# Kernel tuning notes

Hardware: AMD Instinct MI355X
Metric: run time of the kernel (lower is better)

Reference implementation:

```python
import jax, jax.numpy as jnp
import numpy as np

E, M, T, H, V = 512, 1024, 1024, 512, 10000
B, S, L = 16, 80, 200
K = 10  # pooling kernel


def avgpool2d(x, k):
    # torch AvgPool2d(k) on a 3D tensor [B, S, C]: pools over (S, C) with stride k, floor mode
    b, s, c = x.shape
    return x[:, :(s // k) * k, :(c // k) * k].reshape(b, s // k, k, c // k, k).mean(axis=(2, 4))


def lstm(x, h0, c0, Wih, Whh, bih, bhh):
    # torch single-layer LSTM, gate order (i, f, g, o); x: [B, T, H]
    def step(carry, xt):
        h, c = carry
        g = xt @ Wih.T + h @ Whh.T + bih + bhh  # [B, 4H]
        i, f, gg, o = jnp.split(g, 4, axis=-1)
        c = jax.nn.sigmoid(f) * c + jax.nn.sigmoid(i) * jnp.tanh(gg)
        h = jax.nn.sigmoid(o) * jnp.tanh(c)
        return (h, c), h
    (hT, cT), ys = jax.lax.scan(step, (h0, c0), jnp.swapaxes(x, 0, 1))
    return jnp.swapaxes(ys, 0, 1), (hT, cT)


def attend(emb, feats, lens, Ws, bs, hdim):
    # additive score: Linear(cat(emb, feat)) = emb@We.T + feat@Wf.T + b, masked softmax over valid feats
    we, wf = Ws[:, :hdim], Ws[:, hdim:]
    scores = emb @ we.T + jnp.swapaxes(feats @ wf.T, 1, 2) + bs  # [B, S, L]
    mask = jnp.arange(feats.shape[1])[None, None, :] < lens[:, None, None]
    w = jax.nn.softmax(jnp.where(mask, scores, -jnp.inf), axis=-1)
    return jnp.einsum('bsl,blf->bsf', w, feats)


def setup_inputs():
    key = jax.random.key(0)
    ks = jax.random.split(key, 30)
    n = lambda k, shape: jax.random.normal(k, shape, dtype=jnp.float32)
    p = lambda k, shape: 0.02 * jax.random.normal(k, shape, dtype=jnp.float32)
    inp = {
        'mfeat': n(ks[0], (B, L, M)),
        'tfeat': n(ks[1], (B, L, T)),
        'att_motion': n(ks[2], (B, S, M)),
        'att_tempo': n(ks[3], (B, S, T)),
        'embeddings': n(ks[4], (B, S, E)),
        'motion_batch_lens': jax.random.randint(ks[5], (B,), 100, L + 1, dtype=jnp.int32),
        'temp_batch_lens': jax.random.randint(ks[6], (B,), 100, L + 1, dtype=jnp.int32),
        'seq_batch_lens': jnp.full((B,), S, dtype=jnp.int32),
        'Wm': p(ks[7], (M, M)), 'bm': p(ks[8], (M,)),
        'Wt': p(ks[9], (T, T)), 'bt': p(ks[10], (T,)),
        'Wmm': p(ks[11], (H, E + T + M)), 'bmm': p(ks[12], (H,)),
        'Wli': p(ks[13], (H, T // K + M // K)), 'bli': p(ks[14], (H,)),
        'Wih': p(ks[15], (4 * H, H)), 'Whh': p(ks[16], (4 * H, H)),
        'bih': p(ks[17], (4 * H,)), 'bhh': p(ks[18], (4 * H,)),
        'Wsm': p(ks[19], (1, H + M)), 'bsm': p(ks[20], (1,)),
        'Wst': p(ks[21], (1, H + T)), 'bst': p(ks[22], (1,)),
        'Wo': p(ks[23], (V, H + T + M)), 'bo': p(ks[24], (V,)),
    }
    return inp


def reference(mfeat, tfeat, att_motion, att_tempo, embeddings,
              motion_batch_lens, temp_batch_lens, seq_batch_lens,
              Wm, bm, Wt, bt, Wmm, bmm, Wli, bli,
              Wih, Whh, bih, bhh, Wsm, bsm, Wst, bst, Wo, bo):
    # self-gated feature transforms
    temp_mout = att_motion @ Wm.T + bm
    temp_tout = att_tempo @ Wt.T + bt
    temp_mout = temp_mout * jax.nn.softmax(temp_mout, axis=-1)
    temp_tout = temp_tout * jax.nn.softmax(temp_tout, axis=-1)
    # multimodal fusion (dropout = identity in eval)
    mm_inp = jnp.concatenate((embeddings, temp_tout, temp_mout), axis=2)
    mm_out = mm_inp @ Wmm.T + bmm  # [B, S, H]
    # pooled init sequence -> LSTM init hidden
    mean_feat = jnp.concatenate((avgpool2d(att_tempo, K), avgpool2d(att_motion, K)), axis=2)
    m0 = mean_feat @ Wli.T + bli  # [B, S//K, H]
    z = jnp.zeros((att_motion.shape[0], H), dtype=mm_out.dtype)
    _, (h0, c0) = lstm(m0, z, z, Wih, Whh, bih, bhh)
    out, _ = lstm(mm_out, h0, c0, Wih, Whh, bih, bhh)
    act = jnp.tanh(out)
    # ragged additive attention over variable-length video features
    att_m2 = attend(act, mfeat, motion_batch_lens, Wsm, bsm, H)
    att_t2 = attend(act, tfeat, temp_batch_lens, Wst, bst, H)
    final = jnp.concatenate((act, att_t2, att_m2), axis=2) @ Wo.T + bo
    return jax.nn.log_softmax(final, axis=2)
```

## Files before the change

### kernel.cpp

```cpp
#include <hip/hip_runtime.h>
#include <hip/hip_bf16.h>
#include <math.h>


typedef __bf16 bf16x8 __attribute__((ext_vector_type(8)));
typedef float f32x4 __attribute__((ext_vector_type(4)));
typedef unsigned short u16x8 __attribute__((ext_vector_type(8)));

__device__ inline unsigned short f2b(float f){
  union { float f; unsigned u; } v; v.f = f;
  unsigned u = v.u;
  u += 0x7fff + ((u >> 16) & 1);
  return (unsigned short)(u >> 16);
}
__device__ inline float sigm(float x){ return 1.f/(1.f + __expf(-x)); }
__device__ inline float wred_max(float v){ for (int o=32;o;o>>=1) v = fmaxf(v, __shfl_xor(v,o)); return v; }
__device__ inline float wred_sum(float v){ for (int o=32;o;o>>=1) v += __shfl_xor(v,o); return v; }

__device__ inline float bred_max(float v, float* sm){
  v = wred_max(v);
  int w = threadIdx.x >> 6;
  if ((threadIdx.x & 63) == 0) sm[w] = v;
  __syncthreads();
  v = fmaxf(fmaxf(sm[0], sm[1]), fmaxf(sm[2], sm[3]));
  __syncthreads();
  return v;
}
__device__ inline float bred_sum(float v, float* sm){
  v = wred_sum(v);
  int w = threadIdx.x >> 6;
  if ((threadIdx.x & 63) == 0) sm[w] = v;
  __syncthreads();
  v = sm[0] + sm[1] + sm[2] + sm[3];
  __syncthreads();
  return v;
}

#define GLOAD_LDS16(g, l) __builtin_amdgcn_global_load_lds( \
    (const __attribute__((address_space(1))) void*)(g), \
    (__attribute__((address_space(3))) void*)(l), 16, 0, 0)

__global__ void cvt_bf16_kernel(const float* __restrict__ s, unsigned short* __restrict__ d, int n8){
  int i = blockIdx.x*256 + threadIdx.x;
  if (i >= n8) return;
  float4 a = ((const float4*)s)[i*2];
  float4 b = ((const float4*)s)[i*2+1];
  u16x8 o;
  o[0]=f2b(a.x); o[1]=f2b(a.y); o[2]=f2b(a.z); o[3]=f2b(a.w);
  o[4]=f2b(b.x); o[5]=f2b(b.y); o[6]=f2b(b.z); o[7]=f2b(b.w);
  ((u16x8*)d)[i] = o;
}

__global__ void zero_kernel(int* p, int n){
  int i = blockIdx.x*64 + threadIdx.x;
  if (i < n) p[i] = 0;
}

__global__ __launch_bounds__(256) void gemm_bb_kernel(
    const unsigned short* __restrict__ A, const unsigned short* __restrict__ B,
    const float* __restrict__ bias1, const float* __restrict__ bias2,
    float* __restrict__ C, int N, int K)
{
  __shared__ unsigned short lA[128*32];
  __shared__ unsigned short lB[128*32];
  int tid = threadIdx.x;
  int r0 = blockIdx.x << 7, n0 = blockIdx.y << 7;
  int w = tid >> 6, lane = tid & 63;
  int wr = (w >> 1) << 6, wc = (w & 1) << 6;
  int lm = lane & 15, lq = lane >> 4;
  f32x4 acc[4][4] = {};

  int row0 = tid >> 2, row1 = (tid + 256) >> 2, cc = (tid & 3) << 3;
  const unsigned short* Ag0 = A + (size_t)(r0 + row0)*K + cc;
  const unsigned short* Ag1 = A + (size_t)(r0 + row1)*K + cc;
  int br0 = n0 + row0; if (br0 >= N) br0 = N - 1;
  int br1 = n0 + row1; if (br1 >= N) br1 = N - 1;
  const unsigned short* Bg0 = B + (size_t)br0*K + cc;
  const unsigned short* Bg1 = B + (size_t)br1*K + cc;
  unsigned lb0 = (unsigned)(tid & ~63) * 8;
  unsigned lb1 = 2048 + lb0;

  for (int k0 = 0; k0 < K; k0 += 32){
    GLOAD_LDS16(Ag0 + k0, &lA[lb0]);
    GLOAD_LDS16(Ag1 + k0, &lA[lb1]);
    GLOAD_LDS16(Bg0 + k0, &lB[lb0]);
    GLOAD_LDS16(Bg1 + k0, &lB[lb1]);
    __syncthreads();
    bf16x8 af[4], bfr[4];
#pragma unroll
    for (int i=0;i<4;i++){
      af[i]  = *(const bf16x8*)&lA[(wr + i*16 + lm)*32 + lq*8];
      bfr[i] = *(const bf16x8*)&lB[(wc + i*16 + lm)*32 + lq*8];
    }
#pragma unroll
    for (int i=0;i<4;i++)
#pragma unroll
      for (int j=0;j<4;j++)
        acc[i][j] = __builtin_amdgcn_mfma_f32_16x16x32_bf16(af[i], bfr[j], acc[i][j], 0, 0, 0);
    __syncthreads();
  }
#pragma unroll
  for (int i=0;i<4;i++){
    int rbase = r0 + wr + i*16 + lq*4;
#pragma unroll
    for (int j=0;j<4;j++){
      int n = n0 + wc + j*16 + lm;
      if (n < N){
        float bv = (bias1 ? bias1[n] : 0.f) + (bias2 ? bias2[n] : 0.f);
#pragma unroll
        for (int rr=0;rr<4;rr++)
          C[(size_t)(rbase + rr)*N + n] = acc[i][j][rr] + bv;
      }
    }
  }
}

__global__ __launch_bounds__(256) void rowsmx_kernel(const float* __restrict__ X,
    unsigned short* __restrict__ out, int ostride, int ooff)
{
  __shared__ float sm[4];
  int row = blockIdx.x, tid = threadIdx.x;
  const float* xr = X + (size_t)row * 1024;
  float x[4];
#pragma unroll
  for (int j=0;j<4;j++) x[j] = xr[j*256 + tid];
  float m = fmaxf(fmaxf(x[0],x[1]), fmaxf(x[2],x[3]));
  m = bred_max(m, sm);
  float s = 0.f;
#pragma unroll
  for (int j=0;j<4;j++) s += __expf(x[j]-m);
  s = bred_sum(s, sm);
  float inv = 1.f / s;
  unsigned short* o = out + (size_t)row*ostride + ooff;
#pragma unroll
  for (int j=0;j<4;j++) o[j*256 + tid] = f2b(x[j] * (__expf(x[j]-m) * inv));
}

__global__ void embcopy_kernel(const float* __restrict__ emb, unsigned short* __restrict__ mmbf){
  int idx = blockIdx.x*256 + threadIdx.x;
  if (idx >= 1280*64) return;
  int row = idx >> 6, c8 = (idx & 63) << 3;
  const float* s = emb + (size_t)row*512 + c8;
  float4 a = ((const float4*)s)[0], b = ((const float4*)s)[1];
  u16x8 o;
  o[0]=f2b(a.x); o[1]=f2b(a.y); o[2]=f2b(a.z); o[3]=f2b(a.w);
  o[4]=f2b(b.x); o[5]=f2b(b.y); o[6]=f2b(b.z); o[7]=f2b(b.w);
  *(u16x8*)&mmbf[(size_t)row*2560 + c8] = o;
}

__global__ void avgpool_kernel(const float* __restrict__ tempo, const float* __restrict__ motion,
                               float* __restrict__ mf)
{
  int bx = blockIdx.x;
  int c = threadIdx.x;
  if (c >= 204) return;
  int b = bx >> 3, s = bx & 7;
  const float* src = (c < 102) ? (tempo  + ((size_t)(b*80 + s*10))*1024 + c*10)
                               : (motion + ((size_t)(b*80 + s*10))*1024 + (c-102)*10);
  float acc = 0.f;
  for (int r=0;r<10;r++){
    const float* p = src + (size_t)r*1024;
#pragma unroll
    for (int cc=0;cc<10;cc++) acc += p[cc];
  }
  mf[bx*204 + c] = acc * 0.01f;
}

__global__ __launch_bounds__(256) void m0_kernel(const float* __restrict__ mf,
    const float* __restrict__ Wli, const float* __restrict__ bli, float* __restrict__ m0)
{
  __shared__ float rowv[204];
  int bx = blockIdx.x, tid = threadIdx.x;
  if (tid < 204) rowv[tid] = mf[bx*204 + tid];
  __syncthreads();
  for (int c = tid; c < 512; c += 256){
    const float* w = Wli + (size_t)c*204;
    float acc = bli[c];
    for (int k=0;k<204;k++) acc += rowv[k]*w[k];
    m0[bx*512 + c] = acc;
  }
}

#define LSTM_NBLK 32
#define HP 520

__global__ __launch_bounds__(256) void lstm_fused_kernel(
    const float* __restrict__ X1, const float* __restrict__ X2,
    const float* __restrict__ Whh,
    unsigned long long* __restrict__ hb0, unsigned long long* __restrict__ hb1,
    float* __restrict__ finalA, int* __restrict__ bar)
{
  __shared__ unsigned short w_lds[64*HP];
  __shared__ unsigned short h_lds[16*HP];
  __shared__ float gb[4][16][16];
  __shared__ unsigned short hstage[16][16];
  int tid = threadIdx.x, j = blockIdx.x;
  int j16 = j*16;
  int lane = tid & 63, w = tid >> 6;
  int lm = lane & 15, lq = lane >> 4;

  for (int i = 0; i < 16; i++){
    int ch = tid + i*256;
    int r = ch >> 6, c8 = (ch & 63) << 3;
    int grow = (r >> 4)*512 + j16 + (r & 15);
    const float* s = Whh + (size_t)grow*512 + c8;
    float4 a = ((const float4*)s)[0], b = ((const float4*)s)[1];
    u16x8 o;
    o[0]=f2b(a.x); o[1]=f2b(a.y); o[2]=f2b(a.z); o[3]=f2b(a.w);
    o[4]=f2b(b.x); o[5]=f2b(b.y); o[6]=f2b(b.z); o[7]=f2b(b.w);
    *(u16x8*)&w_lds[r*HP + c8] = o;
  }

  float c_reg = 0.f;
  int ul = tid & 15, bb = tid >> 4;
  unsigned long long* hbufs[2] = { hb0, hb1 };
  const int wbase = ((w << 4) + lm)*HP;
  const int abase = lm*HP;
  const int koff = lq << 3;
  int sc = 0;

  for (int seg = 0; seg < 2; seg++){
    const float* Xp = seg ? X2 : X1;
    int Tst = seg ? 80 : 8;
    for (int t = 0; t < Tst; t++){
      if (sc > 0){
        if (tid == 0){
          while (__hip_atomic_load(&bar[sc-1], __ATOMIC_RELAXED, __HIP_MEMORY_SCOPE_AGENT) < LSTM_NBLK)
            __builtin_amdgcn_s_sleep(1);
        }
        __syncthreads();
      }
      size_t xrow = ((size_t)bb*Tst + t)*2048 + j16 + ul;
      float xi = Xp[xrow];
      float xf = Xp[xrow + 512];
      float xg = Xp[xrow + 1024];
      float xo = Xp[xrow + 1536];
      if (sc == 0){
        u16x8 z = {0,0,0,0,0,0,0,0};
        for (int i = tid; i < 1024; i += 256){
          int b = i >> 6, c8 = (i & 63) << 3;
          *(u16x8*)&h_lds[b*HP + c8] = z;
        }
      } else {
        const unsigned long long* src = hbufs[sc & 1];
#pragma unroll
        for (int it = 0; it < 4; it++){
          int i = tid + it*256;
          int b = i >> 6, c64 = i & 63;
          unsigned long long v = __hip_atomic_load(&src[i], __ATOMIC_RELAXED, __HIP_MEMORY_SCOPE_AGENT);
          *(unsigned long long*)&h_lds[b*HP + (c64 << 2)] = v;
        }
      }
      __syncthreads();
      f32x4 a0 = {0.f,0.f,0.f,0.f}, a1 = {0.f,0.f,0.f,0.f};
#pragma unroll
      for (int k0 = 0; k0 < 512; k0 += 64){
        bf16x8 ha = *(const bf16x8*)&h_lds[abase + k0 + koff];
        bf16x8 wa = *(const bf16x8*)&w_lds[wbase + k0 + koff];
        a0 = __builtin_amdgcn_mfma_f32_16x16x32_bf16(ha, wa, a0, 0, 0, 0);
        bf16x8 hbf = *(const bf16x8*)&h_lds[abase + k0 + 32 + koff];
        bf16x8 wbf = *(const bf16x8*)&w_lds[wbase + k0 + 32 + koff];
        a1 = __builtin_amdgcn_mfma_f32_16x16x32_bf16(hbf, wbf, a1, 0, 0, 0);
      }
      f32x4 acc = a0 + a1;
      *(f32x4*)&gb[w][lm][lq << 2] = acc;
      __syncthreads();
      float iv = gb[0][ul][bb] + xi;
      float fv = gb[1][ul][bb] + xf;
      float gv = gb[2][ul][bb] + xg;
      float ov = gb[3][ul][bb] + xo;
      c_reg = sigm(fv)*c_reg + sigm(iv)*tanhf(gv);
      float hn = sigm(ov)*tanhf(c_reg);
      hstage[bb][ul] = f2b(hn);
      if (seg) finalA[(size_t)(bb*80 + t)*2560 + j16 + ul] = tanhf(hn);
      __syncthreads();
      if (tid < 64){
        int b = tid >> 2, ch = tid & 3;
        unsigned long long v = *(const unsigned long long*)&hstage[b][ch << 2];
        unsigned long long* dst = hbufs[(sc + 1) & 1] + (size_t)b*64 + (j16 >> 2) + ch;
        __hip_atomic_store(dst, v, __ATOMIC_RELAXED, __HIP_MEMORY_SCOPE_AGENT);
      }
      sc++;
      __syncthreads();
      if (tid == 0)
        __hip_atomic_fetch_add(&bar[sc-1], 1, __ATOMIC_RELAXED, __HIP_MEMORY_SCOPE_AGENT);
    }
  }
}

__global__ void proj_kernel(const float* __restrict__ A, int stride, int ncols,
                            const float* __restrict__ w, const float* __restrict__ bias,
                            float* __restrict__ out)
{
  int r = blockIdx.x, lane = threadIdx.x;
  const float* a = A + (size_t)r * stride;
  float acc = 0.f;
  for (int c = lane; c < ncols; c += 64) acc += a[c]*w[c];
  acc = wred_sum(acc);
  if (lane == 0) out[r] = acc + (bias ? bias[0] : 0.f);
}

__global__ __launch_bounds__(256) void attsmax_kernel(const float* __restrict__ e,
    const float* __restrict__ f, const int* __restrict__ lens, float* __restrict__ w)
{
  __shared__ float sm[4];
  int bx = blockIdx.x;
  int b = bx / 80;
  int tid = threadIdx.x;
  int len = lens[b];
  bool ok = (tid < 200) && (tid < len);
  float val = ok ? (e[bx] + f[b*200 + tid]) : -1e30f;
  float m = bred_max(val, sm);
  float ex = ok ? __expf(val - m) : 0.f;
  float s = bred_sum(ex, sm);
  if (tid < 200) w[(size_t)bx*200 + tid] = ex / s;
}

__global__ __launch_bounds__(256) void attapply_kernel(const float* __restrict__ w,
    const float* __restrict__ feats, float* __restrict__ finalA, int coloff)
{
  __shared__ float lw[8][200];
  int b = blockIdx.x, sg = blockIdx.y;
  int tid = threadIdx.x;
  for (int i = tid; i < 1600; i += 256){
    int ss = i / 200, l = i - ss*200;
    lw[ss][l] = w[(size_t)(b*80 + sg*8 + ss)*200 + l];
  }
  __syncthreads();
  float4 acc[8];
#pragma unroll
  for (int s=0;s<8;s++) acc[s] = make_float4(0,0,0,0);
  const float* fb = feats + (size_t)b*200*1024 + tid*4;
  for (int l=0;l<200;l++){
    float4 v = *(const float4*)(fb + (size_t)l*1024);
#pragma unroll
    for (int s=0;s<8;s++){
      float wv = lw[s][l];
      acc[s].x += wv*v.x; acc[s].y += wv*v.y; acc[s].z += wv*v.z; acc[s].w += wv*v.w;
    }
  }
#pragma unroll
  for (int s=0;s<8;s++){
    float* o = finalA + (size_t)(b*80 + sg*8 + s)*2560 + coloff + tid*4;
    *(float4*)o = acc[s];
  }
}

__global__ __launch_bounds__(256) void logsmax_kernel(float* __restrict__ out)
{
  __shared__ float buf[10000];
  __shared__ float sm[4];
  int row = blockIdx.x, tid = threadIdx.x;
  float* o = out + (size_t)row * 10000;
  float m = -1e30f;
  for (int i = tid; i < 10000; i += 256){ float v = o[i]; buf[i] = v; m = fmaxf(m, v); }
  m = bred_max(m, sm);
  float s = 0.f;
  for (int i = tid; i < 10000; i += 256) s += __expf(buf[i] - m);
  s = bred_sum(s, sm);
  float lse = m + __logf(s);
  for (int i = tid; i < 10000; i += 256) o[i] = buf[i] - lse;
}

extern "C" void kernel_launch(void* const* d_in, const int* in_sizes, int n_in,
                              void* d_out, int out_size, void* d_ws, size_t ws_size,
                              hipStream_t stream)
{
  const float* mfeat = (const float*)d_in[0];
  const float* tfeat = (const float*)d_in[1];
  const float* attm  = (const float*)d_in[2];
  const float* attt  = (const float*)d_in[3];
  const float* emb   = (const float*)d_in[4];
  const int* lens_m  = (const int*)d_in[5];
  const int* lens_t  = (const int*)d_in[6];
  const float* Wm  = (const float*)d_in[8];
  const float* bm  = (const float*)d_in[9];
  const float* Wt  = (const float*)d_in[10];
  const float* bt  = (const float*)d_in[11];
  const float* Wmm = (const float*)d_in[12];
  const float* bmm = (const float*)d_in[13];
  const float* Wli = (const float*)d_in[14];
  const float* bli = (const float*)d_in[15];
  const float* Wih = (const float*)d_in[16];
  const float* Whh = (const float*)d_in[17];
  const float* bih = (const float*)d_in[18];
  const float* bhh = (const float*)d_in[19];
  const float* Wsm = (const float*)d_in[20];
  const float* bsm = (const float*)d_in[21];
  const float* Wst = (const float*)d_in[22];
  const float* bst = (const float*)d_in[23];
  const float* Wo  = (const float*)d_in[24];
  const float* bo  = (const float*)d_in[25];
  float* out = (float*)d_out;

  char* ws = (char*)d_ws;
  size_t off = 0;
  auto alloc = [&](size_t bytes)->void* {
    void* p = (void*)(ws + off);
    off += (bytes + 255) & ~(size_t)255;
    return p;
  };
  float* finalA = (float*)alloc(1280UL*2560*4);
  float* moutp  = (float*)alloc(1280UL*1024*4);
  float* toutp  = (float*)alloc(1280UL*1024*4);
  float* mm_out = (float*)alloc(1280UL*512*4);
  float* meanf  = (float*)alloc(128UL*204*4);
  float* m0     = (float*)alloc(128UL*512*4);
  float* X1     = (float*)alloc(128UL*2048*4);
  float* X2     = (float*)alloc(1280UL*2048*4);
  float* e_m = (float*)alloc(1280UL*4); float* e_t = (float*)alloc(1280UL*4);
  float* f_m = (float*)alloc(3200UL*4); float* f_t = (float*)alloc(3200UL*4);
  float* w_m = (float*)alloc(1280UL*200*4); float* w_t = (float*)alloc(1280UL*200*4);
  int* bar = (int*)alloc(128*4);
  unsigned long long* hbuf0 = (unsigned long long*)alloc(16UL*512*2);
  unsigned long long* hbuf1 = (unsigned long long*)alloc(16UL*512*2);
  unsigned short* attm_bf   = (unsigned short*)alloc(1280UL*1024*2);
  unsigned short* attt_bf   = (unsigned short*)alloc(1280UL*1024*2);
  unsigned short* Wm_bf     = (unsigned short*)alloc(1024UL*1024*2);
  unsigned short* Wt_bf     = (unsigned short*)alloc(1024UL*1024*2);
  unsigned short* Wmm_bf    = (unsigned short*)alloc(512UL*2560*2);
  unsigned short* Wih_bf    = (unsigned short*)alloc(2048UL*512*2);
  unsigned short* Wo_bf     = (unsigned short*)alloc(10000UL*2560*2);
  unsigned short* mm_inp_bf = (unsigned short*)alloc(1280UL*2560*2);
  unsigned short* mm_out_bf = (unsigned short*)alloc(1280UL*512*2);
  unsigned short* m0_bf     = (unsigned short*)alloc(128UL*512*2);
  unsigned short* finalA_bf = (unsigned short*)alloc(1280UL*2560*2);

  auto cvt = [&](const float* s, unsigned short* d, size_t n){
    int n8 = (int)(n/8);
    cvt_bf16_kernel<<<(n8 + 255)/256, 256, 0, stream>>>(s, d, n8);
  };
  cvt(attm, attm_bf, 1280UL*1024);
  cvt(attt, attt_bf, 1280UL*1024);
  cvt(Wm,  Wm_bf,  1024UL*1024);
  cvt(Wt,  Wt_bf,  1024UL*1024);
  cvt(Wmm, Wmm_bf, 512UL*2560);
  cvt(Wih, Wih_bf, 2048UL*512);
  cvt(Wo,  Wo_bf,  10000UL*2560);
  zero_kernel<<<2, 64, 0, stream>>>(bar, 128);

  gemm_bb_kernel<<<dim3(10, 8), 256, 0, stream>>>(attm_bf, Wm_bf, bm, nullptr, moutp, 1024, 1024);
  gemm_bb_kernel<<<dim3(10, 8), 256, 0, stream>>>(attt_bf, Wt_bf, bt, nullptr, toutp, 1024, 1024);
  rowsmx_kernel<<<1280, 256, 0, stream>>>(moutp, mm_inp_bf, 2560, 1536);
  rowsmx_kernel<<<1280, 256, 0, stream>>>(toutp, mm_inp_bf, 2560, 512);
  embcopy_kernel<<<(1280*64 + 255)/256, 256, 0, stream>>>(emb, mm_inp_bf);
  gemm_bb_kernel<<<dim3(10, 4), 256, 0, stream>>>(mm_inp_bf, Wmm_bf, bmm, nullptr, mm_out, 512, 2560);
  cvt(mm_out, mm_out_bf, 1280UL*512);
  avgpool_kernel<<<128, 256, 0, stream>>>(attt, attm, meanf);
  m0_kernel<<<128, 256, 0, stream>>>(meanf, Wli, bli, m0);
  cvt(m0, m0_bf, 128UL*512);
  gemm_bb_kernel<<<dim3(1, 16), 256, 0, stream>>>(m0_bf, Wih_bf, bih, bhh, X1, 2048, 512);
  gemm_bb_kernel<<<dim3(10, 16), 256, 0, stream>>>(mm_out_bf, Wih_bf, bih, bhh, X2, 2048, 512);
  lstm_fused_kernel<<<LSTM_NBLK, 256, 0, stream>>>(X1, X2, Whh, hbuf0, hbuf1, finalA, bar);
  proj_kernel<<<1280, 64, 0, stream>>>(finalA, 2560, 512, Wsm, bsm, e_m);
  proj_kernel<<<3200, 64, 0, stream>>>(mfeat, 1024, 1024, Wsm + 512, nullptr, f_m);
  proj_kernel<<<1280, 64, 0, stream>>>(finalA, 2560, 512, Wst, bst, e_t);
  proj_kernel<<<3200, 64, 0, stream>>>(tfeat, 1024, 1024, Wst + 512, nullptr, f_t);
  attsmax_kernel<<<1280, 256, 0, stream>>>(e_t, f_t, lens_t, w_t);
  attsmax_kernel<<<1280, 256, 0, stream>>>(e_m, f_m, lens_m, w_m);
  attapply_kernel<<<dim3(16,10), 256, 0, stream>>>(w_t, tfeat, finalA, 512);
  attapply_kernel<<<dim3(16,10), 256, 0, stream>>>(w_m, mfeat, finalA, 1536);
  cvt(finalA, finalA_bf, 1280UL*2560);
  gemm_bb_kernel<<<dim3(10, 79), 256, 0, stream>>>(finalA_bf, Wo_bf, bo, nullptr, out, 10000, 2560);
  logsmax_kernel<<<1280, 256, 0, stream>>>(out);
}
```

Before: 1.044 ms.

## Use per-wave flag barriers and wave-local gate layout in fused LSTM

Reorders the Whh rows each block keeps in LDS so that every wave holds all four gates for four hidden units. Each wave can then apply the cell update from its own MFMA output without block-wide syncs. The shared atomic counter barrier becomes per-step, per-wave flags that every lane polls, h is packed with shuffles and published per wave, and the h LDS buffer is double-buffered. tanhf is also replaced with an exp-based fast tanh. This targets per-timestep latency in the serial recurrence, at the cost of more flag memory, more polling traffic, and slightly different tanh accuracy.

```diff
diff --git a/kernel.cpp b/kernel.cpp
--- a/kernel.cpp
+++ b/kernel.cpp
@@ -14,6 +14,10 @@
   return (unsigned short)(u >> 16);
 }
 __device__ inline float sigm(float x){ return 1.f/(1.f + __expf(-x)); }
+__device__ inline float tanh_fast(float x){
+  float e = __expf(2.f*x);
+  return 1.f - 2.f/(e + 1.f);
+}
 __device__ inline float wred_max(float v){ for (int o=32;o;o>>=1) v = fmaxf(v, __shfl_xor(v,o)); return v; }
 __device__ inline float wred_sum(float v){ for (int o=32;o;o>>=1) v += __shfl_xor(v,o); return v; }
 
@@ -191,18 +195,18 @@
     float* __restrict__ finalA, int* __restrict__ bar)
 {
   __shared__ unsigned short w_lds[64*HP];
-  __shared__ unsigned short h_lds[16*HP];
-  __shared__ float gb[4][16][16];
-  __shared__ unsigned short hstage[16][16];
+  __shared__ unsigned short h_lds[2][16*HP];
+  __shared__ float gbw[4][16][20];
   int tid = threadIdx.x, j = blockIdx.x;
   int j16 = j*16;
   int lane = tid & 63, w = tid >> 6;
   int lm = lane & 15, lq = lane >> 4;
+  int bc = lane >> 2, uu = lane & 3, ul = (w << 2) + uu;
 
   for (int i = 0; i < 16; i++){
     int ch = tid + i*256;
     int r = ch >> 6, c8 = (ch & 63) << 3;
-    int grow = (r >> 4)*512 + j16 + (r & 15);
+    int grow = ((r >> 2) & 3)*512 + j16 + ((r >> 4) << 2) + (r & 3);
     const float* s = Whh + (size_t)grow*512 + c8;
     float4 a = ((const float4*)s)[0], b = ((const float4*)s)[1];
     u16x8 o;
@@ -210,10 +214,15 @@
     o[4]=f2b(b.x); o[5]=f2b(b.y); o[6]=f2b(b.z); o[7]=f2b(b.w);
     *(u16x8*)&w_lds[r*HP + c8] = o;
   }
+  {
+    u16x8 z = {0,0,0,0,0,0,0,0};
+    for (int i = tid; i < 1024; i += 256){
+      int b = i >> 6, c8 = (i & 63) << 3;
+      *(u16x8*)&h_lds[0][b*HP + c8] = z;
+    }
+  }
 
   float c_reg = 0.f;
-  int ul = tid & 15, bb = tid >> 4;
-  unsigned long long* hbufs[2] = { hb0, hb1 };
   const int wbase = ((w << 4) + lm)*HP;
   const int abase = lm*HP;
   const int koff = lq << 3;
@@ -222,68 +231,65 @@
   for (int seg = 0; seg < 2; seg++){
     const float* Xp = seg ? X2 : X1;
     int Tst = seg ? 80 : 8;
-    for (int t = 0; t < Tst; t++){
-      if (sc > 0){
-        if (tid == 0){
-          while (__hip_atomic_load(&bar[sc-1], __ATOMIC_RELAXED, __HIP_MEMORY_SCOPE_AGENT) < LSTM_NBLK)
-            __builtin_amdgcn_s_sleep(1);
-        }
-        __syncthreads();
-      }
-      size_t xrow = ((size_t)bb*Tst + t)*2048 + j16 + ul;
+    for (int t = 0; t < Tst; t++, sc++){
+      bool last = (seg == 1) && (t == Tst - 1);
+      size_t xrow = ((size_t)bc*Tst + t)*2048 + j16 + ul;
       float xi = Xp[xrow];
       float xf = Xp[xrow + 512];
       float xg = Xp[xrow + 1024];
       float xo = Xp[xrow + 1536];
-      if (sc == 0){
-        u16x8 z = {0,0,0,0,0,0,0,0};
-        for (int i = tid; i < 1024; i += 256){
-          int b = i >> 6, c8 = (i & 63) << 3;
-          *(u16x8*)&h_lds[b*HP + c8] = z;
-        }
-      } else {
-        const unsigned long long* src = hbufs[sc & 1];
-#pragma unroll
-        for (int it = 0; it < 4; it++){
+      if (sc > 0){
+        const int* fp = bar + (sc - 1)*128;
+        while (__hip_atomic_load(&fp[lane], __ATOMIC_RELAXED, __HIP_MEMORY_SCOPE_AGENT) == 0)
+          __builtin_amdgcn_s_sleep(1);
+        while (__hip_atomic_load(&fp[lane + 64], __ATOMIC_RELAXED, __HIP_MEMORY_SCOPE_AGENT) == 0)
+          __builtin_amdgcn_s_sleep(1);
+        asm volatile("" ::: "memory");
+        const unsigned long long* src = (sc & 1) ? hb1 : hb0;
+        unsigned short* hb = &h_lds[sc & 1][0];
+#pragma unroll
+        for (int it = 0; it < 8; it++){
           int i = tid + it*256;
-          int b = i >> 6, c64 = i & 63;
+          int b = i >> 7, c64 = i & 127;
           unsigned long long v = __hip_atomic_load(&src[i], __ATOMIC_RELAXED, __HIP_MEMORY_SCOPE_AGENT);
-          *(unsigned long long*)&h_lds[b*HP + (c64 << 2)] = v;
+          *(unsigned long long*)&hb[b*HP + (c64 << 2)] = v;
         }
       }
       __syncthreads();
+      const unsigned short* hrow = &h_lds[sc & 1][abase];
       f32x4 a0 = {0.f,0.f,0.f,0.f}, a1 = {0.f,0.f,0.f,0.f};
 #pragma unroll
       for (int k0 = 0; k0 < 512; k0 += 64){
-        bf16x8 ha = *(const bf16x8*)&h_lds[abase + k0 + koff];
+        bf16x8 ha = *(const bf16x8*)&hrow[k0 + koff];
         bf16x8 wa = *(const bf16x8*)&w_lds[wbase + k0 + koff];
         a0 = __builtin_amdgcn_mfma_f32_16x16x32_bf16(ha, wa, a0, 0, 0, 0);
-        bf16x8 hbf = *(const bf16x8*)&h_lds[abase + k0 + 32 + koff];
+        bf16x8 hbf = *(const bf16x8*)&hrow[k0 + 32 + koff];
         bf16x8 wbf = *(const bf16x8*)&w_lds[wbase + k0 + 32 + koff];
         a1 = __builtin_amdgcn_mfma_f32_16x16x32_bf16(hbf, wbf, a1, 0, 0, 0);
       }
-      f32x4 acc = a0 + a1;
-      *(f32x4*)&gb[w][lm][lq << 2] = acc;
-      __syncthreads();
-      float iv = gb[0][ul][bb] + xi;
-      float fv = gb[1][ul][bb] + xf;
-      float gv = gb[2][ul][bb] + xg;
-      float ov = gb[3][ul][bb] + xo;
-      c_reg = sigm(fv)*c_reg + sigm(iv)*tanhf(gv);
-      float hn = sigm(ov)*tanhf(c_reg);
-      hstage[bb][ul] = f2b(hn);
-      if (seg) finalA[(size_t)(bb*80 + t)*2560 + j16 + ul] = tanhf(hn);
-      __syncthreads();
-      if (tid < 64){
-        int b = tid >> 2, ch = tid & 3;
-        unsigned long long v = *(const unsigned long long*)&hstage[b][ch << 2];
-        unsigned long long* dst = hbufs[(sc + 1) & 1] + (size_t)b*64 + (j16 >> 2) + ch;
-        __hip_atomic_store(dst, v, __ATOMIC_RELAXED, __HIP_MEMORY_SCOPE_AGENT);
+      *(f32x4*)&gbw[w][lm][lq << 2] = a0 + a1;
+      float iv = gbw[w][uu     ][bc] + xi;
+      float fv = gbw[w][4 + uu ][bc] + xf;
+      float gv = gbw[w][8 + uu ][bc] + xg;
+      float ov = gbw[w][12 + uu][bc] + xo;
+      c_reg = sigm(fv)*c_reg + sigm(iv)*tanh_fast(gv);
+      float hn = sigm(ov)*tanh_fast(c_reg);
+      if (seg) finalA[(size_t)(bc*80 + t)*2560 + j16 + ul] = tanh_fast(hn);
+      if (!last){
+        unsigned hv = (unsigned)f2b(hn);
+        unsigned p = (hv & 0xffffu) | ((unsigned)__shfl_xor((int)hv, 1) << 16);
+        unsigned q = (unsigned)__shfl_xor((int)p, 2);
+        if ((lane & 3) == 0){
+          unsigned long long v64 = ((unsigned long long)q << 32) | (unsigned long long)p;
+          unsigned long long* dstb = ((sc + 1) & 1) ? hb1 : hb0;
+          __hip_atomic_store(dstb + (size_t)bc*128 + (j << 2) + w, v64,
+                             __ATOMIC_RELAXED, __HIP_MEMORY_SCOPE_AGENT);
+        }
+        asm volatile("s_waitcnt vmcnt(0)" ::: "memory");
+        if (lane == 0)
+          __hip_atomic_store(&bar[sc*128 + (j << 2) + w], 1,
+                             __ATOMIC_RELAXED, __HIP_MEMORY_SCOPE_AGENT);
       }
-      sc++;
-      __syncthreads();
-      if (tid == 0)
-        __hip_atomic_fetch_add(&bar[sc-1], 1, __ATOMIC_RELAXED, __HIP_MEMORY_SCOPE_AGENT);
     }
   }
 }
@@ -411,7 +417,7 @@
   float* e_m = (float*)alloc(1280UL*4); float* e_t = (float*)alloc(1280UL*4);
   float* f_m = (float*)alloc(3200UL*4); float* f_t = (float*)alloc(3200UL*4);
   float* w_m = (float*)alloc(1280UL*200*4); float* w_t = (float*)alloc(1280UL*200*4);
-  int* bar = (int*)alloc(128*4);
+  int* bar = (int*)alloc(88UL*128*4);
   unsigned long long* hbuf0 = (unsigned long long*)alloc(16UL*512*2);
   unsigned long long* hbuf1 = (unsigned long long*)alloc(16UL*512*2);
   unsigned short* attm_bf   = (unsigned short*)alloc(1280UL*1024*2);
@@ -437,7 +443,7 @@
   cvt(Wmm, Wmm_bf, 512UL*2560);
   cvt(Wih, Wih_bf, 2048UL*512);
   cvt(Wo,  Wo_bf,  10000UL*2560);
-  zero_kernel<<<2, 64, 0, stream>>>(bar, 128);
+  zero_kernel<<<(88*128 + 63)/64, 64, 0, stream>>>(bar, 88*128);
 
   gemm_bb_kernel<<<dim3(10, 8), 256, 0, stream>>>(attm_bf, Wm_bf, bm, nullptr, moutp, 1024, 1024);
   gemm_bb_kernel<<<dim3(10, 8), 256, 0, stream>>>(attt_bf, Wt_bf, bt, nullptr, toutp, 1024, 1024);
```

Measured after the change: 1.284 ms. 1.23x slower.

## Overlap Wo bf16 conversion and feature projections with LSTM via extra blocks

Applied to the files above, without the earlier changes.

Launches 224 extra blocks alongside the 32 recurrent LSTM blocks. They convert Wo to bf16 and compute the mfeat/tfeat score projections while the latency-bound recurrence runs on otherwise idle CUs. The LSTM and attapply kernels now write bf16 finalA directly, which drops a separate conversion pass. Paired GEMMs and row-softmax launches are merged into single launches. The hidden-state exchange now reads the full 512-wide row, which the old loop did not. Extra blocks could compete for scheduling with the spin-barrier LSTM blocks.

```diff
diff --git a/kernel.cpp b/kernel.cpp
--- a/kernel.cpp
+++ b/kernel.cpp
@@ -56,13 +56,12 @@
   if (i < n) p[i] = 0;
 }
 
-__global__ __launch_bounds__(256) void gemm_bb_kernel(
+__device__ __forceinline__ void gemm_body(
     const unsigned short* __restrict__ A, const unsigned short* __restrict__ B,
     const float* __restrict__ bias1, const float* __restrict__ bias2,
-    float* __restrict__ C, int N, int K)
-{
-  __shared__ unsigned short lA[128*32];
-  __shared__ unsigned short lB[128*32];
+    float* __restrict__ C, int N, int K,
+    unsigned short* lA, unsigned short* lB)
+{
   int tid = threadIdx.x;
   int r0 = blockIdx.x << 7, n0 = blockIdx.y << 7;
   int w = tid >> 6, lane = tid & 63;
@@ -115,12 +114,36 @@
   }
 }
 
-__global__ __launch_bounds__(256) void rowsmx_kernel(const float* __restrict__ X,
-    unsigned short* __restrict__ out, int ostride, int ooff)
+__global__ __launch_bounds__(256) void gemm_bb_kernel(
+    const unsigned short* __restrict__ A, const unsigned short* __restrict__ B,
+    const float* __restrict__ bias1, const float* __restrict__ bias2,
+    float* __restrict__ C, int N, int K)
+{
+  __shared__ unsigned short lA[128*32];
+  __shared__ unsigned short lB[128*32];
+  gemm_body(A, B, bias1, bias2, C, N, K, lA, lB);
+}
+
+__global__ __launch_bounds__(256) void gemm_bb2_kernel(
+    const unsigned short* __restrict__ A0, const unsigned short* __restrict__ B0,
+    const float* __restrict__ b0, float* __restrict__ C0,
+    const unsigned short* __restrict__ A1, const unsigned short* __restrict__ B1,
+    const float* __restrict__ b1, float* __restrict__ C1, int N, int K)
+{
+  __shared__ unsigned short lA[128*32];
+  __shared__ unsigned short lB[128*32];
+  if (blockIdx.z == 0) gemm_body(A0, B0, b0, nullptr, C0, N, K, lA, lB);
+  else                 gemm_body(A1, B1, b1, nullptr, C1, N, K, lA, lB);
+}
+
+__global__ __launch_bounds__(256) void rowsmx2_kernel(const float* __restrict__ X0,
+    const float* __restrict__ X1, unsigned short* __restrict__ out)
 {
   __shared__ float sm[4];
-  int row = blockIdx.x, tid = threadIdx.x;
-  const float* xr = X + (size_t)row * 1024;
+  int bx = blockIdx.x, tid = threadIdx.x;
+  int row = (bx < 1280) ? bx : bx - 1280;
+  const float* xr = ((bx < 1280) ? X0 : X1) + (size_t)row * 1024;
+  int ooff = (bx < 1280) ? 1536 : 512;
   float x[4];
 #pragma unroll
   for (int j=0;j<4;j++) x[j] = xr[j*256 + tid];
@@ -131,7 +154,7 @@
   for (int j=0;j<4;j++) s += __expf(x[j]-m);
   s = bred_sum(s, sm);
   float inv = 1.f / s;
-  unsigned short* o = out + (size_t)row*ostride + ooff;
+  unsigned short* o = out + (size_t)row*2560 + ooff;
 #pragma unroll
   for (int j=0;j<4;j++) o[j*256 + tid] = f2b(x[j] * (__expf(x[j]-m) * inv));
 }
@@ -188,13 +211,42 @@
     const float* __restrict__ X1, const float* __restrict__ X2,
     const float* __restrict__ Whh,
     unsigned long long* __restrict__ hb0, unsigned long long* __restrict__ hb1,
-    float* __restrict__ finalA, int* __restrict__ bar)
+    float* __restrict__ finalA, unsigned short* __restrict__ finalA_bf,
+    int* __restrict__ bar,
+    const float* __restrict__ Wo, unsigned short* __restrict__ Wo_bf,
+    const float* __restrict__ mfeat, const float* __restrict__ tfeat,
+    const float* __restrict__ Wsm, const float* __restrict__ Wst,
+    float* __restrict__ f_m, float* __restrict__ f_t)
 {
   __shared__ unsigned short w_lds[64*HP];
   __shared__ unsigned short h_lds[16*HP];
   __shared__ float gb[4][16][16];
   __shared__ unsigned short hstage[16][16];
   int tid = threadIdx.x, j = blockIdx.x;
+
+  if (j >= LSTM_NBLK){
+    int hb = j - LSTM_NBLK;
+    for (int ch = hb*256 + tid; ch < 3200000; ch += 224*256){
+      float4 a = ((const float4*)Wo)[ch*2];
+      float4 b = ((const float4*)Wo)[ch*2+1];
+      u16x8 o;
+      o[0]=f2b(a.x); o[1]=f2b(a.y); o[2]=f2b(a.z); o[3]=f2b(a.w);
+      o[4]=f2b(b.x); o[5]=f2b(b.y); o[6]=f2b(b.z); o[7]=f2b(b.w);
+      ((u16x8*)Wo_bf)[ch] = o;
+    }
+    int wv = hb*4 + (tid >> 6);
+    int lane = tid & 63;
+    for (int r = wv; r < 6400; r += 896){
+      const float* a = (r < 3200) ? (mfeat + (size_t)r*1024) : (tfeat + (size_t)(r-3200)*1024);
+      const float* wvec = (r < 3200) ? (Wsm + 512) : (Wst + 512);
+      float acc = 0.f;
+      for (int c = lane; c < 1024; c += 64) acc += a[c]*wvec[c];
+      acc = wred_sum(acc);
+      if (lane == 0){ if (r < 3200) f_m[r] = acc; else f_t[r-3200] = acc; }
+    }
+    return;
+  }
+
   int j16 = j*16;
   int lane = tid & 63, w = tid >> 6;
   int lm = lane & 15, lq = lane >> 4;
@@ -244,9 +296,9 @@
       } else {
         const unsigned long long* src = hbufs[sc & 1];
 #pragma unroll
-        for (int it = 0; it < 4; it++){
+        for (int it = 0; it < 8; it++){
           int i = tid + it*256;
-          int b = i >> 6, c64 = i & 63;
+          int b = i >> 7, c64 = i & 127;
           unsigned long long v = __hip_atomic_load(&src[i], __ATOMIC_RELAXED, __HIP_MEMORY_SCOPE_AGENT);
           *(unsigned long long*)&h_lds[b*HP + (c64 << 2)] = v;
         }
@@ -272,12 +324,17 @@
       c_reg = sigm(fv)*c_reg + sigm(iv)*tanhf(gv);
       float hn = sigm(ov)*tanhf(c_reg);
       hstage[bb][ul] = f2b(hn);
-      if (seg) finalA[(size_t)(bb*80 + t)*2560 + j16 + ul] = tanhf(hn);
+      if (seg){
+        float act = tanhf(hn);
+        size_t fo = (size_t)(bb*80 + t)*2560 + j16 + ul;
+        finalA[fo] = act;
+        finalA_bf[fo] = f2b(act);
+      }
       __syncthreads();
       if (tid < 64){
         int b = tid >> 2, ch = tid & 3;
         unsigned long long v = *(const unsigned long long*)&hstage[b][ch << 2];
-        unsigned long long* dst = hbufs[(sc + 1) & 1] + (size_t)b*64 + (j16 >> 2) + ch;
+        unsigned long long* dst = hbufs[(sc + 1) & 1] + (size_t)b*128 + (j << 2) + ch;
         __hip_atomic_store(dst, v, __ATOMIC_RELAXED, __HIP_MEMORY_SCOPE_AGENT);
       }
       sc++;
@@ -317,7 +374,7 @@
 }
 
 __global__ __launch_bounds__(256) void attapply_kernel(const float* __restrict__ w,
-    const float* __restrict__ feats, float* __restrict__ finalA, int coloff)
+    const float* __restrict__ feats, unsigned short* __restrict__ finalA_bf, int coloff)
 {
   __shared__ float lw[8][200];
   int b = blockIdx.x, sg = blockIdx.y;
@@ -341,8 +398,9 @@
   }
 #pragma unroll
   for (int s=0;s<8;s++){
-    float* o = finalA + (size_t)(b*80 + sg*8 + s)*2560 + coloff + tid*4;
-    *(float4*)o = acc[s];
+    ushort4 o;
+    o.x = f2b(acc[s].x); o.y = f2b(acc[s].y); o.z = f2b(acc[s].z); o.w = f2b(acc[s].w);
+    *(ushort4*)&finalA_bf[(size_t)(b*80 + sg*8 + s)*2560 + coloff + tid*4] = o;
   }
 }
 
@@ -412,8 +470,8 @@
   float* f_m = (float*)alloc(3200UL*4); float* f_t = (float*)alloc(3200UL*4);
   float* w_m = (float*)alloc(1280UL*200*4); float* w_t = (float*)alloc(1280UL*200*4);
   int* bar = (int*)alloc(128*4);
-  unsigned long long* hbuf0 = (unsigned long long*)alloc(16UL*512*2);
-  unsigned long long* hbuf1 = (unsigned long long*)alloc(16UL*512*2);
+  unsigned long long* hbuf0 = (unsigned long long*)alloc(16UL*128*8);
+  unsigned long long* hbuf1 = (unsigned long long*)alloc(16UL*128*8);
   unsigned short* attm_bf   = (unsigned short*)alloc(1280UL*1024*2);
   unsigned short* attt_bf   = (unsigned short*)alloc(1280UL*1024*2);
   unsigned short* Wm_bf     = (unsigned short*)alloc(1024UL*1024*2);
@@ -436,13 +494,11 @@
   cvt(Wt,  Wt_bf,  1024UL*1024);
   cvt(Wmm, Wmm_bf, 512UL*2560);
   cvt(Wih, Wih_bf, 2048UL*512);
-  cvt(Wo,  Wo_bf,  10000UL*2560);
   zero_kernel<<<2, 64, 0, stream>>>(bar, 128);
 
-  gemm_bb_kernel<<<dim3(10, 8), 256, 0, stream>>>(attm_bf, Wm_bf, bm, nullptr, moutp, 1024, 1024);
-  gemm_bb_kernel<<<dim3(10, 8), 256, 0, stream>>>(attt_bf, Wt_bf, bt, nullptr, toutp, 1024, 1024);
-  rowsmx_kernel<<<1280, 256, 0, stream>>>(moutp, mm_inp_bf, 2560, 1536);
-  rowsmx_kernel<<<1280, 256, 0, stream>>>(toutp, mm_inp_bf, 2560, 512);
+  gemm_bb2_kernel<<<dim3(10, 8, 2), 256, 0, stream>>>(
+      attm_bf, Wm_bf, bm, moutp, attt_bf, Wt_bf, bt, toutp, 1024, 1024);
+  rowsmx2_kernel<<<2560, 256, 0, stream>>>(moutp, toutp, mm_inp_bf);
   embcopy_kernel<<<(1280*64 + 255)/256, 256, 0, stream>>>(emb, mm_inp_bf);
   gemm_bb_kernel<<<dim3(10, 4), 256, 0, stream>>>(mm_inp_bf, Wmm_bf, bmm, nullptr, mm_out, 512, 2560);
   cvt(mm_out, mm_out_bf, 1280UL*512);
@@ -451,16 +507,14 @@
   cvt(m0, m0_bf, 128UL*512);
   gemm_bb_kernel<<<dim3(1, 16), 256, 0, stream>>>(m0_bf, Wih_bf, bih, bhh, X1, 2048, 512);
   gemm_bb_kernel<<<dim3(10, 16), 256, 0, stream>>>(mm_out_bf, Wih_bf, bih, bhh, X2, 2048, 512);
-  lstm_fused_kernel<<<LSTM_NBLK, 256, 0, stream>>>(X1, X2, Whh, hbuf0, hbuf1, finalA, bar);
+  lstm_fused_kernel<<<256, 256, 0, stream>>>(X1, X2, Whh, hbuf0, hbuf1,
+      finalA, finalA_bf, bar, Wo, Wo_bf, mfeat, tfeat, Wsm, Wst, f_m, f_t);
   proj_kernel<<<1280, 64, 0, stream>>>(finalA, 2560, 512, Wsm, bsm, e_m);
-  proj_kernel<<<3200, 64, 0, stream>>>(mfeat, 1024, 1024, Wsm + 512, nullptr, f_m);
   proj_kernel<<<1280, 64, 0, stream>>>(finalA, 2560, 512, Wst, bst, e_t);
-  proj_kernel<<<3200, 64, 0, stream>>>(tfeat, 1024, 1024, Wst + 512, nullptr, f_t);
   attsmax_kernel<<<1280, 256, 0, stream>>>(e_t, f_t, lens_t, w_t);
   attsmax_kernel<<<1280, 256, 0, stream>>>(e_m, f_m, lens_m, w_m);
-  attapply_kernel<<<dim3(16,10), 256, 0, stream>>>(w_t, tfeat, finalA, 512);
-  attapply_kernel<<<dim3(16,10), 256, 0, stream>>>(w_m, mfeat, finalA, 1536);
-  cvt(finalA, finalA_bf, 1280UL*2560);
+  attapply_kernel<<<dim3(16,10), 256, 0, stream>>>(w_t, tfeat, finalA_bf, 512);
+  attapply_kernel<<<dim3(16,10), 256, 0, stream>>>(w_m, mfeat, finalA_bf, 1536);
   gemm_bb_kernel<<<dim3(10, 79), 256, 0, stream>>>(finalA_bf, Wo_bf, bo, nullptr, out, 10000, 2560);
   logsmax_kernel<<<1280, 256, 0, stream>>>(out);
 }
```

After: 1.028 ms. No clear change (-1.6%).
